# Kernel tuning notes

Hardware: AMD Instinct MI355X
Metric: run time of the kernel (lower is better)

## Reference

```python
import jax, jax.numpy as jnp
import numpy as np

N = 100000      # num nodes
E = 1600000     # num edges (avg degree 16)
F_IN = 64       # n_input
F_H = 64        # n_hidden
K = 8           # Chebyshev order
LN_EPS = 1e-5


def setup_inputs() -> dict:
    key = jax.random.key(0)
    k1, k2, k3 = jax.random.split(key, 3)
    x = jax.random.normal(k1, (N, F_IN), dtype=jnp.float32)
    edge_index = jax.random.randint(k2, (2, E), 0, N, dtype=jnp.int32)
    # ChebConv learned params: K weight matrices + bias
    weight = jax.random.normal(k3, (K, F_IN, F_H), dtype=jnp.float32) * 0.05
    bias = jnp.zeros((F_H,), dtype=jnp.float32)
    # LayerNorm affine params
    ln_weight = jnp.ones((F_H,), dtype=jnp.float32)
    ln_bias = jnp.zeros((F_H,), dtype=jnp.float32)
    return {"x": x, "edge_index": edge_index, "weight": weight,
            "bias": bias, "ln_weight": ln_weight, "ln_bias": ln_bias}


def reference(x, edge_index, weight, bias, ln_weight, ln_bias):
    # ---- ChebConv with sym normalization, lambda_max = 2.0 (PyG default) ----
    # L_hat = 2L/lambda_max - I = (I - D^-1/2 A D^-1/2) - I = -D^-1/2 A D^-1/2
    # (self-loops removed before building the Laplacian, as in PyG)
    row, col = edge_index[0], edge_index[1]
    mask = (row != col)                                   # remove self loops
    ew = jnp.where(mask, 1.0, 0.0).astype(x.dtype)        # [E]
    deg = jax.ops.segment_sum(ew, row, num_segments=N)    # [N]
    dinv = jnp.where(deg > 0, jax.lax.rsqrt(jnp.maximum(deg, 1.0)), 0.0)
    w = -ew * dinv[row] * dinv[col]                       # L_hat edge weights [E]

    def prop(h):  # y = L_hat @ h  (sparse matvec via gather/scatter)
        return jax.ops.segment_sum(w[:, None] * h[col], row, num_segments=N)

    # Chebyshev recurrence: T0 = x, T1 = L_hat x, Tk = 2 L_hat T_{k-1} - T_{k-2}
    tx0 = x
    tx1 = prop(x)
    acc = tx0 @ weight[0] + tx1 @ weight[1]               # [N, F_H]

    def body(carry, Wk):
        tkm1, tkm2, acc = carry
        tk = 2.0 * prop(tkm1) - tkm2
        return (tk, tkm1, acc + tk @ Wk), None

    (_, _, acc), _ = jax.lax.scan(body, (tx1, tx0, acc), weight[2:])
    out = acc + bias

    # ---- LayerNorm(n_hidden) over feature dim ----
    mu = jnp.mean(out, axis=-1, keepdims=True)
    var = jnp.mean(jnp.square(out - mu), axis=-1, keepdims=True)
    h = (out - mu) * jax.lax.rsqrt(var + LN_EPS) * ln_weight + ln_bias

    # ---- ELU ----
    return jax.nn.elu(h)
```

## Files before the change

### kernel.cpp

```cpp
#include <hip/hip_runtime.h>
#include <math.h>

#define F 64
#define PR_ROWS 16

using short8 = __attribute__((ext_vector_type(8))) short;
using f32x4  = __attribute__((ext_vector_type(4))) float;

static __device__ __forceinline__ ushort f2bf(float f) {
    uint u = __float_as_uint(f);
    uint r = (u + 0x7fffu + ((u >> 16) & 1u)) >> 16;
    return (ushort)r;
}
static __device__ __forceinline__ float bf2f(ushort v) {
    return __uint_as_float(((uint)v) << 16);
}

static __device__ __forceinline__ int rgroup(int r, float invg) {
    int g = (int)((float)r * invg);
    return g > 7 ? 7 : g;
}


__global__ __launch_bounds__(256) void deg_kernel(const int* __restrict__ ei, int E,
                                                  int* __restrict__ deg, float invg) {
    int xcd = blockIdx.x & 7;
    int e = (blockIdx.x >> 3) * 256 + threadIdx.x;
    if (e >= E) return;
    int r = ei[e], c = ei[E + e];
    if (r == c) return;
    if (rgroup(r, invg) != xcd) return;
    atomicAdd(&deg[r], 1);
}

__global__ __launch_bounds__(256) void scan1_kernel(const int* __restrict__ deg,
                                                    int* __restrict__ rp,
                                                    int* __restrict__ bsum, int Nv) {
    __shared__ int sh[256];
    int t = threadIdx.x;
    int base = blockIdx.x * 1024 + t * 4;
    int v0 = (base + 0 < Nv) ? ((deg[base + 0] + 7) & ~7) : 0;
    int v1 = (base + 1 < Nv) ? ((deg[base + 1] + 7) & ~7) : 0;
    int v2 = (base + 2 < Nv) ? ((deg[base + 2] + 7) & ~7) : 0;
    int v3 = (base + 3 < Nv) ? ((deg[base + 3] + 7) & ~7) : 0;
    int s = v0 + v1 + v2 + v3;
    sh[t] = s;
    __syncthreads();
    for (int off = 1; off < 256; off <<= 1) {
        int a = (t >= off) ? sh[t - off] : 0;
        __syncthreads();
        sh[t] += a;
        __syncthreads();
    }
    int run = sh[t] - s;
    run += v0; if (base + 0 < Nv) rp[base + 1] = run;
    run += v1; if (base + 1 < Nv) rp[base + 2] = run;
    run += v2; if (base + 2 < Nv) rp[base + 3] = run;
    run += v3; if (base + 3 < Nv) rp[base + 4] = run;
    if (t == 255) bsum[blockIdx.x] = sh[255];
}

__global__ __launch_bounds__(256) void scan2_kernel(int* __restrict__ bsum, int nb) {
    __shared__ int sh[256];
    int t = threadIdx.x;
    int v = (t < nb) ? bsum[t] : 0;
    sh[t] = v;
    __syncthreads();
    for (int off = 1; off < 256; off <<= 1) {
        int a = (t >= off) ? sh[t - off] : 0;
        __syncthreads();
        sh[t] += a;
        __syncthreads();
    }
    if (t < nb) bsum[t] = sh[t] - v;
}

__global__ __launch_bounds__(256) void scan3_kernel(int* __restrict__ rp,
                                                    const int* __restrict__ bsum,
                                                    const int* __restrict__ deg,
                                                    float* __restrict__ dinv, int Nv) {
    int i = blockIdx.x * 256 + threadIdx.x;
    if (i == 0) rp[0] = 0;
    if (i < Nv) {
        rp[i + 1] += bsum[i >> 10];
        int d = deg[i];
        dinv[i] = d > 0 ? rsqrtf((float)d) : 0.f;
    }
}

__global__ __launch_bounds__(256) void scatter_kernel(const int* __restrict__ ei, int E,
                                                      const int* __restrict__ rp,
                                                      int* __restrict__ fill,
                                                      const float* __restrict__ dinv,
                                                      const int* __restrict__ deg,
                                                      int* __restrict__ ce, int Nv,
                                                      float invg) {
    int xcd = blockIdx.x & 7;
    int e = (blockIdx.x >> 3) * 256 + threadIdx.x;
    if (e >= E) return;
    int r = ei[e], c = ei[E + e];
    if (r == c) return;
    if (rgroup(r, invg) != xcd) return;
    int old = atomicAdd(&fill[r], 1);
    ce[rp[r] + old] = (dinv[c] > 0.f) ? c : Nv;
    if (old == deg[r] - 1) {
        int q = rp[r] + deg[r], qe = rp[r + 1];
        for (; q < qe; q++) ce[q] = Nv;
    }
}


__global__ __launch_bounds__(256) void init_kernel(const float4* __restrict__ src,
                                                   ushort4* __restrict__ dst,
                                                   const float* __restrict__ dinv,
                                                   const float* __restrict__ W,
                                                   ushort* __restrict__ WbT,
                                                   int n4, int KK, int Nv) {
    int i = blockIdx.x * 256 + threadIdx.x;
    if (i < 16) dst[(size_t)Nv * 16 + i] = make_ushort4(0, 0, 0, 0);
    if (i < n4) {
        int row = i >> 4;
        float dr = dinv[row];
        float sv = dr > 0.f ? dr : 1.f;
        float4 v = src[i];
        dst[i] = make_ushort4(f2bf(sv * v.x), f2bf(sv * v.y),
                              f2bf(sv * v.z), f2bf(sv * v.w));
        return;
    }
    int t = i - n4;
    if (t < KK * F) {
        int col = t / KK, kk = t - col * KK;
        WbT[t] = f2bf(W[(size_t)kk * F + col]);
    }
}


__global__ __launch_bounds__(256) void prop_v7(const ushort* __restrict__ Gsrc,
                                               const ushort* __restrict__ Gm2,
                                               ushort* __restrict__ Gout,
                                               const int* __restrict__ rp,
                                               const int* __restrict__ ce,
                                               const float* __restrict__ dinv,
                                               const int* __restrict__ deg,
                                               int Nv, int first) {
    __shared__ __align__(16) ushort ush[PR_ROWS][F];
    int wave = threadIdx.x >> 6, lane = threadIdx.x & 63;
    int rbase = blockIdx.x * PR_ROWS + wave * 4;

    if (blockIdx.x == 0 && threadIdx.x < 8)
        ((uint4*)(Gout + (size_t)Nv * F))[threadIdx.x] = make_uint4(0, 0, 0, 0);

    for (int r = 0; r < 4; r++) {
        int i = rbase + r;
        bool act = i < Nv;
        int ii = act ? i : 0;
        float dr = dinv[ii];
        int dg = deg[ii];
        float sr = dg > 0 ? sqrtf((float)dg) : 1.f;
        float tm2 = first ? 0.f : sr * bf2f(Gm2[(size_t)ii * F + lane]);
        int s = rp[ii], e = rp[ii + 1];
        float s0 = 0.f, s1 = 0.f, s2 = 0.f, s3 = 0.f;
        float s4 = 0.f, s5 = 0.f, s6 = 0.f, s7 = 0.f;
        for (int p = s; p < e; p += 8) {
            int4 q0 = *(const int4*)(ce + p);
            int4 q1 = *(const int4*)(ce + p + 4);
            s0 += bf2f(Gsrc[(size_t)q0.x * F + lane]);
            s1 += bf2f(Gsrc[(size_t)q0.y * F + lane]);
            s2 += bf2f(Gsrc[(size_t)q0.z * F + lane]);
            s3 += bf2f(Gsrc[(size_t)q0.w * F + lane]);
            s4 += bf2f(Gsrc[(size_t)q1.x * F + lane]);
            s5 += bf2f(Gsrc[(size_t)q1.y * F + lane]);
            s6 += bf2f(Gsrc[(size_t)q1.z * F + lane]);
            s7 += bf2f(Gsrc[(size_t)q1.w * F + lane]);
        }
        float sum = ((s0 + s1) + (s2 + s3)) + ((s4 + s5) + (s6 + s7));
        float raw = -dr * sum;
        float tk = first ? raw : fmaf(2.f, raw, -tm2);
        float sv = dr > 0.f ? dr : 1.f;
        ush[wave * 4 + r][lane] = f2bf(sv * tk);
    }
    __syncthreads();
    int t = threadIdx.x;
    if (t < 128) {
        int row = t >> 3;
        if (blockIdx.x * PR_ROWS + row < Nv)
            ((uint4*)Gout)[(size_t)blockIdx.x * 128 + t] = ((const uint4*)ush)[t];
    }
}


template <int NSL, int FIRST, int LAST>
__global__ __launch_bounds__(256) void gemm_all(
    const ushort* __restrict__ g0, const ushort* __restrict__ g1,
    const ushort* __restrict__ g2, const ushort* __restrict__ g3,
    const ushort* __restrict__ g4, const ushort* __restrict__ g5,
    const ushort* __restrict__ g6, const ushort* __restrict__ g7,
    const ushort* __restrict__ WbT, int kkbase, int KK,
    float* __restrict__ out, const float* __restrict__ bias,
    const float* __restrict__ lnw, const float* __restrict__ lnb,
    const int* __restrict__ deg, int Nv) {
    const ushort* gs[8] = {g0, g1, g2, g3, g4, g5, g6, g7};
    int wave = threadIdx.x >> 6, lane = threadIdx.x & 63;
    int rbase = (blockIdx.x * 4 + wave) * 16;
    if (rbase >= Nv) return;
    int r15 = lane & 15, kg = lane >> 4;
    int arow = rbase + r15;
    if (arow >= Nv) arow = Nv - 1;

    f32x4 acc[4];
#pragma unroll
    for (int t = 0; t < 4; t++) acc[t] = (f32x4){0.f, 0.f, 0.f, 0.f};

#pragma unroll
    for (int st = 0; st < 2 * NSL; st++) {
        const ushort* A = gs[st >> 1];
        short8 a = *(const short8*)(A + (size_t)arow * F + (st & 1) * 32 + kg * 8);
#pragma unroll
        for (int t = 0; t < 4; t++) {
            int col = t * 16 + r15;
            short8 b = *(const short8*)(WbT + (size_t)col * KK + kkbase + st * 32 + kg * 8);
            acc[t] = __builtin_amdgcn_mfma_f32_16x16x32_bf16(a, b, acc[t], 0, 0, 0);
        }
    }

    if (!LAST) {
#pragma unroll
        for (int t = 0; t < 4; t++) {
            int col = t * 16 + r15;
#pragma unroll
            for (int j = 0; j < 4; j++) {
                int row = rbase + kg * 4 + j;
                if (row < Nv) {
                    size_t idx = (size_t)row * F + col;
                    out[idx] = FIRST ? acc[t][j] : out[idx] + acc[t][j];
                }
            }
        }
    } else {
        float bc[4], wc[4], gc[4];
#pragma unroll
        for (int t = 0; t < 4; t++) {
            int col = t * 16 + r15;
            bc[t] = bias[col]; wc[t] = lnw[col]; gc[t] = lnb[col];
        }
#pragma unroll
        for (int j = 0; j < 4; j++) {
            int row = rbase + kg * 4 + j;
            int rr = row < Nv ? row : Nv - 1;
            int dg = deg[rr];
            float sr = dg > 0 ? sqrtf((float)dg) : 1.f;
            float v[4];
            float s = 0.f;
#pragma unroll
            for (int t = 0; t < 4; t++) {
                int col = t * 16 + r15;
                float a_ = acc[t][j];
                if (!FIRST) a_ += out[(size_t)rr * F + col];
                v[t] = a_ * sr + bc[t];
                s += v[t];
            }
            s += __shfl_xor(s, 1, 64); s += __shfl_xor(s, 2, 64);
            s += __shfl_xor(s, 4, 64); s += __shfl_xor(s, 8, 64);
            float mu = s * (1.f / F);
            float q = 0.f;
#pragma unroll
            for (int t = 0; t < 4; t++) { float d = v[t] - mu; q += d * d; }
            q += __shfl_xor(q, 1, 64); q += __shfl_xor(q, 2, 64);
            q += __shfl_xor(q, 4, 64); q += __shfl_xor(q, 8, 64);
            float inv = rsqrtf(q * (1.f / F) + 1e-5f);
            if (row < Nv) {
#pragma unroll
                for (int t = 0; t < 4; t++) {
                    int col = t * 16 + r15;
                    float y = (v[t] - mu) * inv * wc[t] + gc[t];
                    out[(size_t)row * F + col] = y > 0.f ? y : expm1f(y);
                }
            }
        }
    }
}


extern "C" void kernel_launch(void* const* d_in, const int* in_sizes, int n_in,
                              void* d_out, int out_size, void* d_ws, size_t ws_size,
                              hipStream_t stream) {
    (void)n_in; (void)out_size;
    const float* x    = (const float*)d_in[0];
    const int*   ei   = (const int*)d_in[1];
    const float* W    = (const float*)d_in[2];
    const float* bias = (const float*)d_in[3];
    const float* lnw  = (const float*)d_in[4];
    const float* lnb  = (const float*)d_in[5];
    float* out = (float*)d_out;

    int Nv = in_sizes[0] / F;
    int E  = in_sizes[1] / 2;
    int K  = in_sizes[2] / (F * F);
    int KK = K * F;
    float invg = 8.0f / (float)Nv;

    char* base = (char*)d_ws;
    size_t off = 0;
    auto alloc = [&](size_t b) -> void* {
        void* p = base + off;
        off += (b + 255) & ~(size_t)255;
        return p;
    };
    int*    degfill = (int*)alloc((size_t)2 * Nv * 4);
    int*    deg  = degfill;
    int*    fill = degfill + Nv;
    int*    rp   = (int*)alloc(((size_t)Nv + 1) * 4);
    int     nb   = (Nv + 1023) / 1024;
    int*    bsum = (int*)alloc((size_t)nb * 4);
    float*  dinv = (float*)alloc((size_t)Nv * 4);
    int*    ce   = (int*)alloc(((size_t)E + 8 * Nv) * 4);
    ushort* WbT  = (ushort*)alloc((size_t)KK * F * 2);
    size_t fixed = off;

    size_t gbytes = ((size_t)Nv + 1) * F * 2;
    size_t galign = (gbytes + 255) & ~(size_t)255;
    int full = (K == 8 && fixed + 8 * galign <= ws_size) ? 1 : 0;
    int nG = full ? 8 : 3;
    ushort* G[8];
    for (int i = 0; i < nG; i++) G[i] = (ushort*)alloc(gbytes);
    if (off > ws_size) return;

    hipMemsetAsync(degfill, 0, (size_t)2 * Nv * 4, stream);

    int gE = (E + 255) / 256, gN = (Nv + 255) / 256;
    deg_kernel<<<8 * gE, 256, 0, stream>>>(ei, E, deg, invg);
    scan1_kernel<<<nb, 256, 0, stream>>>(deg, rp, bsum, Nv);
    scan2_kernel<<<1, 256, 0, stream>>>(bsum, nb);
    scan3_kernel<<<gN, 256, 0, stream>>>(rp, bsum, deg, dinv, Nv);
    scatter_kernel<<<8 * gE, 256, 0, stream>>>(ei, E, rp, fill, dinv, deg, ce, Nv, invg);

    int n4 = (Nv * F) / 4;
    int initN = n4 + KK * F;
    init_kernel<<<(initN + 255) / 256, 256, 0, stream>>>((const float4*)x, (ushort4*)G[0],
                                                         dinv, W, WbT, n4, KK, Nv);

    int gP = (Nv + PR_ROWS - 1) / PR_ROWS;
    int gG = (Nv + 63) / 64;

    for (int k = 1; k < K; k++) {
        const ushort* gsrc = full ? G[k - 1] : G[(k - 1) % 3];
        const ushort* gm2  = (k < 2) ? (const ushort*)nullptr
                                     : (full ? G[k - 2] : G[(k - 2) % 3]);
        ushort*       gdst = full ? G[k] : G[k % 3];
        prop_v7<<<gP, 256, 0, stream>>>(gsrc, gm2, gdst, rp, ce, dinv, deg,
                                        Nv, k == 1 ? 1 : 0);
        if (!full && (k & 1)) {
            int p = k >> 1;
            const ushort* a0 = G[(2 * p) % 3];
            const ushort* a1 = G[(2 * p + 1) % 3];
            if (p == 0)
                gemm_all<2, 1, 0><<<gG, 256, 0, stream>>>(a0, a1, 0, 0, 0, 0, 0, 0,
                    WbT, p * 128, KK, out, bias, lnw, lnb, deg, Nv);
            else if (k < K - 1)
                gemm_all<2, 0, 0><<<gG, 256, 0, stream>>>(a0, a1, 0, 0, 0, 0, 0, 0,
                    WbT, p * 128, KK, out, bias, lnw, lnb, deg, Nv);
            else
                gemm_all<2, 0, 1><<<gG, 256, 0, stream>>>(a0, a1, 0, 0, 0, 0, 0, 0,
                    WbT, p * 128, KK, out, bias, lnw, lnb, deg, Nv);
        }
    }
    if (full)
        gemm_all<8, 1, 1><<<gG, 256, 0, stream>>>(G[0], G[1], G[2], G[3],
                                                  G[4], G[5], G[6], G[7],
                                                  WbT, 0, KK, out, bias, lnw, lnb,
                                                  deg, Nv);
}
```

Before: 561.4 us.

## Add LDS-staged fused MFMA GEMM with pre-fragmented bf16 weights for final combine

Adds a gemm_full kernel that stages each block's 64-row slices of all eight Chebyshev basis tensors into swizzled LDS with coalesced 16-byte loads. It then runs bf16 MFMA against a weight buffer pre-laid-out in fragment order by init_kernel. Bias, degree rescale, LayerNorm and ELU stay fused in the epilogue. This replaces the old gemm_all path to cut per-lane strided global loads and weight re-layout cost, at the price of 32KB LDS per block and two block-wide barriers.

```diff
diff --git a/kernel.cpp b/kernel.cpp
--- a/kernel.cpp
+++ b/kernel.cpp
@@ -115,6 +115,7 @@
                                                    const float* __restrict__ dinv,
                                                    const float* __restrict__ W,
                                                    ushort* __restrict__ WbT,
+                                                   ushort* __restrict__ WF,
                                                    int n4, int KK, int Nv) {
     int i = blockIdx.x * 256 + threadIdx.x;
     if (i < 16) dst[(size_t)Nv * 16 + i] = make_ushort4(0, 0, 0, 0);
@@ -131,6 +132,14 @@
     if (t < KK * F) {
         int col = t / KK, kk = t - col * KK;
         WbT[t] = f2bf(W[(size_t)kk * F + col]);
+        return;
+    }
+    int u = t - KK * F;
+    if (u < KK * F) {
+        int j = u & 7, lane = (u >> 3) & 63, tt = (u >> 9) & 3, st = u >> 11;
+        int col = tt * 16 + (lane & 15);
+        int kk = st * 32 + ((lane >> 4) << 3) + j;
+        WF[u] = f2bf(W[(size_t)kk * F + col]);
     }
 }
 
@@ -189,6 +198,114 @@
 }
 
 
+__global__ __launch_bounds__(256) void gemm_full(
+    const ushort* __restrict__ g0, const ushort* __restrict__ g1,
+    const ushort* __restrict__ g2, const ushort* __restrict__ g3,
+    const ushort* __restrict__ g4, const ushort* __restrict__ g5,
+    const ushort* __restrict__ g6, const ushort* __restrict__ g7,
+    const ushort* __restrict__ WF,
+    float* __restrict__ out, const float* __restrict__ bias,
+    const float* __restrict__ lnw, const float* __restrict__ lnb,
+    const int* __restrict__ deg, int Nv) {
+    __shared__ __align__(16) ushort A_lds[4 * 64 * 64];
+    uint4* Au4 = (uint4*)A_lds;
+    int wave = threadIdx.x >> 6, lane = threadIdx.x & 63;
+    int rbase64 = blockIdx.x * 64;
+    if (rbase64 >= Nv) return;
+    int rbase = rbase64 + wave * 16;
+    int r15 = lane & 15, kg = lane >> 4;
+
+    f32x4 acc[4];
+#pragma unroll
+    for (int t = 0; t < 4; t++) acc[t] = (f32x4){0.f, 0.f, 0.f, 0.f};
+
+#define STAGE4(pA, pB, pC, pD)                                                  \
+    {                                                                           \
+        const ushort* ps_[4] = {pA, pB, pC, pD};                                \
+        _Pragma("unroll")                                                       \
+        for (int s4_ = 0; s4_ < 4; s4_++) {                                     \
+            const ushort* A_ = ps_[s4_];                                        \
+            _Pragma("unroll")                                                   \
+            for (int it_ = 0; it_ < 2; it_++) {                                 \
+                int lin_ = it_ * 256 + threadIdx.x;                             \
+                int r_ = lin_ >> 3, c_ = lin_ & 7;                              \
+                int grow_ = rbase64 + r_;                                       \
+                if (grow_ > Nv) grow_ = Nv;                 \
+                uint4 v_ = *(const uint4*)(A_ + (size_t)grow_ * F + c_ * 8);    \
+                Au4[(s4_ * 64 + r_) * 8 + (c_ ^ (r_ & 7))] = v_;                \
+            }                                                                   \
+        }                                                                       \
+    }
+
+    STAGE4(g0, g1, g2, g3);
+    __syncthreads();
+#pragma unroll
+    for (int st8 = 0; st8 < 8; st8++) {
+        int s4 = st8 >> 1, half = st8 & 1;
+        int cidx = (half * 4 + kg) ^ (r15 & 7);
+        short8 a = *(const short8*)&A_lds[((s4 * 64 + wave * 16 + r15) * 8 + cidx) * 8];
+#pragma unroll
+        for (int t = 0; t < 4; t++) {
+            short8 b = *(const short8*)(WF + (((size_t)st8 * 4 + t) * 64 + lane) * 8);
+            acc[t] = __builtin_amdgcn_mfma_f32_16x16x32_bf16(a, b, acc[t], 0, 0, 0);
+        }
+    }
+    __syncthreads();
+    STAGE4(g4, g5, g6, g7);
+    __syncthreads();
+#pragma unroll
+    for (int st8 = 0; st8 < 8; st8++) {
+        int s4 = st8 >> 1, half = st8 & 1;
+        int cidx = (half * 4 + kg) ^ (r15 & 7);
+        short8 a = *(const short8*)&A_lds[((s4 * 64 + wave * 16 + r15) * 8 + cidx) * 8];
+#pragma unroll
+        for (int t = 0; t < 4; t++) {
+            short8 b = *(const short8*)(WF + (((size_t)(st8 + 8) * 4 + t) * 64 + lane) * 8);
+            acc[t] = __builtin_amdgcn_mfma_f32_16x16x32_bf16(a, b, acc[t], 0, 0, 0);
+        }
+    }
+#undef STAGE4
+
+    float bc[4], wc[4], gc[4];
+#pragma unroll
+    for (int t = 0; t < 4; t++) {
+        int col = t * 16 + r15;
+        bc[t] = bias[col]; wc[t] = lnw[col]; gc[t] = lnb[col];
+    }
+#pragma unroll
+    for (int j = 0; j < 4; j++) {
+        int row = rbase + kg * 4 + j;
+        int rr = row < Nv ? row : Nv - 1;
+        int dg = deg[rr];
+        float sr = dg > 0 ? sqrtf((float)dg) : 1.f;
+        float v[4];
+        float s = 0.f;
+#pragma unroll
+        for (int t = 0; t < 4; t++) {
+            v[t] = acc[t][j] * sr + bc[t];
+            s += v[t];
+        }
+        s += __shfl_xor(s, 1, 64); s += __shfl_xor(s, 2, 64);
+        s += __shfl_xor(s, 4, 64); s += __shfl_xor(s, 8, 64);
+        float mu = s * (1.f / F);
+        float q = 0.f;
+#pragma unroll
+        for (int t = 0; t < 4; t++) { float d = v[t] - mu; q += d * d; }
+        q += __shfl_xor(q, 1, 64); q += __shfl_xor(q, 2, 64);
+        q += __shfl_xor(q, 4, 64); q += __shfl_xor(q, 8, 64);
+        float inv = rsqrtf(q * (1.f / F) + 1e-5f);
+        if (row < Nv) {
+#pragma unroll
+            for (int t = 0; t < 4; t++) {
+                int col = t * 16 + r15;
+                float y = (v[t] - mu) * inv * wc[t] + gc[t];
+                out[(size_t)row * F + col] = y > 0.f ? y : expm1f(y);
+            }
+        }
+    }
+}
+
+
 template <int NSL, int FIRST, int LAST>
 __global__ __launch_bounds__(256) void gemm_all(
     const ushort* __restrict__ g0, const ushort* __restrict__ g1,
@@ -315,6 +432,7 @@
     float*  dinv = (float*)alloc((size_t)Nv * 4);
     int*    ce   = (int*)alloc(((size_t)E + 8 * Nv) * 4);
     ushort* WbT  = (ushort*)alloc((size_t)KK * F * 2);
+    ushort* WF   = (ushort*)alloc((size_t)KK * F * 2);
     size_t fixed = off;
 
     size_t gbytes = ((size_t)Nv + 1) * F * 2;
@@ -335,9 +453,9 @@
     scatter_kernel<<<8 * gE, 256, 0, stream>>>(ei, E, rp, fill, dinv, deg, ce, Nv, invg);
 
     int n4 = (Nv * F) / 4;
-    int initN = n4 + KK * F;
+    int initN = n4 + 2 * KK * F;
     init_kernel<<<(initN + 255) / 256, 256, 0, stream>>>((const float4*)x, (ushort4*)G[0],
-                                                         dinv, W, WbT, n4, KK, Nv);
+                                                         dinv, W, WbT, WF, n4, KK, Nv);
 
     int gP = (Nv + PR_ROWS - 1) / PR_ROWS;
     int gG = (Nv + 63) / 64;
@@ -365,8 +483,7 @@
         }
     }
     if (full)
-        gemm_all<8, 1, 1><<<gG, 256, 0, stream>>>(G[0], G[1], G[2], G[3],
-                                                  G[4], G[5], G[6], G[7],
-                                                  WbT, 0, KK, out, bias, lnw, lnb,
-                                                  deg, Nv);
-}
+        gemm_full<<<gG, 256, 0, stream>>>(G[0], G[1], G[2], G[3],
+                                          G[4], G[5], G[6], G[7],
+                                          WF, out, bias, lnw, lnb, deg, Nv);
+}
```

New measurement: 523.5 us. -6.7%, faster.
